# Optimization experiments

Hardware: AMD Instinct MI355X
Metric: run time of the kernel (lower is better)

Reference implementation:

```python
import jax, jax.numpy as jnp
import numpy as np

N_NODES = 100000
N_EDGES = 1600000
IN_CH = 1024
FEAT_CH = 128
OUT_CH = 3


def setup_inputs() -> dict:
    key = jax.random.key(0)
    ks = jax.random.split(key, 9)
    features = jax.random.normal(ks[0], (N_NODES, IN_CH), dtype=jnp.float32)
    edges = jax.random.randint(ks[1], (2, N_EDGES), 0, N_NODES, dtype=jnp.int64)
    edges2 = jax.random.randint(ks[2], (2, N_EDGES), 0, N_NODES, dtype=jnp.int64)
    edge_features = jax.random.normal(ks[3], (N_EDGES, 1), dtype=jnp.float32)
    additional_feature = jax.random.normal(ks[4], (N_NODES, 20), dtype=jnp.float32)
    # GCNConv linear weights (glorot-ish scale) and biases
    W1 = jax.random.normal(ks[5], (IN_CH, FEAT_CH), dtype=jnp.float32) * (1.0 / np.sqrt(IN_CH))
    b1 = jnp.zeros((FEAT_CH,), dtype=jnp.float32)
    W2 = jax.random.normal(ks[6], (FEAT_CH, OUT_CH), dtype=jnp.float32) * (1.0 / np.sqrt(FEAT_CH))
    b2 = jnp.zeros((OUT_CH,), dtype=jnp.float32)
    return {"features": features, "edges": edges, "edges2": edges2,
            "edge_features": edge_features, "additional_feature": additional_feature,
            "W1": W1, "b1": b1, "W2": W2, "b2": b2}


def gcn_conv(x, edge_index, W, b, num_nodes):
    """PyG GCNConv: x' = D^{-1/2}(A+I)D^{-1/2} x W + b (self-loops added)."""
    x = x @ W  # project first (cheaper feature dim for aggregation)
    loop = jnp.arange(num_nodes, dtype=edge_index.dtype)
    src = jnp.concatenate([edge_index[0], loop])
    dst = jnp.concatenate([edge_index[1], loop])
    deg = jax.ops.segment_sum(jnp.ones_like(dst, dtype=x.dtype), dst,
                              num_segments=num_nodes)  # >=1 due to self-loops
    dinv = jax.lax.rsqrt(deg)
    norm = dinv[src] * dinv[dst]  # [E+N]
    out = jax.ops.segment_sum(x[src] * norm[:, None], dst, num_segments=num_nodes)
    return out + b


def reference(features, edges, edges2, edge_features, additional_feature, W1, b1, W2, b2):
    # use_additional_channels=False -> features unchanged; edge_features forced to None
    n = features.shape[0]
    x = gcn_conv(features, edges2, W1, b1, n)
    x = jax.nn.relu(x)
    # dropout inactive in eval mode
    return gcn_conv(x, edges2, W2, b2, n)
```

## Files before the change

### kernel.cpp

```cpp
#include <hip/hip_runtime.h>
#include <hip/hip_bf16.h>

typedef __attribute__((ext_vector_type(8))) _Float16 half8;
typedef __attribute__((ext_vector_type(4))) float f32x4;

#define N_NODES 100000
#define N_EDGES 1600000
#define IN_CH 1024
#define FEAT 128
#define CAP 64
#define NDIG 196
#define CAPC 10240
#define NGB ((N_NODES + 127) / 128)

__device__ __forceinline__ void gload16(const void* g, void* l) {
    __builtin_amdgcn_global_load_lds(
        (const __attribute__((address_space(1))) unsigned int*)g,
        (__attribute__((address_space(3))) unsigned int*)l, 16, 0, 0);
}

#define WAITV(n)                                                               \
    do {                                                                       \
        asm volatile("s_waitcnt vmcnt(" #n ")" ::: "memory");                  \
        __builtin_amdgcn_sched_barrier(0);                                     \
    } while (0)

__global__ void k_prep(const float* __restrict__ W1, _Float16* __restrict__ Bf,
                       int* __restrict__ cursorC, int* __restrict__ done) {
    int idx = blockIdx.x * 256 + threadIdx.x;
    if (idx < IN_CH * FEAT) {
        int col = idx & (FEAT - 1), k = idx >> 7;
        int cf = col >> 4, s = k >> 5;
        int lane = ((k >> 3) & 3) * 16 + (col & 15);
        int e = k & 7;
        Bf[(((cf * 32 + s) * 64 + lane) << 3) + e] = (_Float16)W1[idx];
    }
    if (idx < NDIG) cursorC[idx] = idx * CAPC;
    if (idx == 0) *done = 0;
}

__global__ __launch_bounds__(256, 2) void k_build_gemm(
    const float* __restrict__ A, const _Float16* __restrict__ Bf,
    const int4* __restrict__ src4, const int4* __restrict__ dst4,
    int* __restrict__ cursorC, uint2* __restrict__ recs,
    int* __restrict__ csr, int* __restrict__ cnt, float* __restrict__ dinvarr,
    int* __restrict__ done, _Float16* __restrict__ H, int M, int e4)
{
    __shared__ union {
        float As[16384];
        struct { int hist[NDIG], segoff[NDIG], lcur[NDIG]; } bin;
        int cl[512];
    } sm;
    const int t = threadIdx.x;

    if (blockIdx.x < NDIG) {
        const int b = blockIdx.x;
        if (t < NDIG) sm.bin.hist[t] = 0;
        __syncthreads();
        const int base4 = b * 2048;
        int4 sv[8], dv[8];
#pragma unroll
        for (int j = 0; j < 8; ++j) {
            int idx = base4 + j * 256 + t;
            if (idx < e4) { sv[j] = src4[idx]; dv[j] = dst4[idx]; }
            else { sv[j] = (int4){-1,-1,-1,-1}; dv[j] = (int4){-1,-1,-1,-1}; }
        }
#pragma unroll
        for (int j = 0; j < 8; ++j) {
            int dd[4] = {dv[j].x, dv[j].y, dv[j].z, dv[j].w};
            int ss[4] = {sv[j].x, sv[j].y, sv[j].z, sv[j].w};
#pragma unroll
            for (int c = 0; c < 4; ++c)
                if ((unsigned)dd[c] < N_NODES && (unsigned)ss[c] < N_NODES)
                    atomicAdd(&sm.bin.hist[dd[c] >> 9], 1);
        }
        __syncthreads();
        if (t < NDIG) {
            sm.bin.segoff[t] = atomicAdd(&cursorC[t], sm.bin.hist[t]);
            sm.bin.lcur[t] = 0;
        }
        __syncthreads();
#pragma unroll
        for (int j = 0; j < 8; ++j) {
            int dd[4] = {dv[j].x, dv[j].y, dv[j].z, dv[j].w};
            int ss[4] = {sv[j].x, sv[j].y, sv[j].z, sv[j].w};
#pragma unroll
            for (int c = 0; c < 4; ++c) {
                if ((unsigned)dd[c] < N_NODES && (unsigned)ss[c] < N_NODES) {
                    int dg = dd[c] >> 9;
                    int r = atomicAdd(&sm.bin.lcur[dg], 1);
                    int pos = sm.bin.segoff[dg] + r;
                    if (pos < (dg + 1) * CAPC)
                        recs[pos] = (uint2){(unsigned)ss[c], (unsigned)dd[c]};
                }
            }
        }
        __syncthreads();
        if (t == 0) {
            __threadfence();
            __hip_atomic_fetch_add(done, 1, __ATOMIC_RELEASE, __HIP_MEMORY_SCOPE_AGENT);
            while (__hip_atomic_load(done, __ATOMIC_ACQUIRE, __HIP_MEMORY_SCOPE_AGENT) < NDIG)
                __builtin_amdgcn_s_sleep(8);
        }
        __syncthreads();
        const int d = blockIdx.x;
        for (int j = t; j < 512; j += 256) sm.cl[j] = 0;
        __syncthreads();
        const int base = d * CAPC;
        int n = cursorC[d] - base;
        if (n > CAPC) n = CAPC;
        for (int k = t; k < n; k += 256) {
            uint2 r = recs[base + k];
            int local = (int)r.y & 511;
            int slot = atomicAdd(&sm.cl[local], 1);
            if (slot < CAP) csr[((int)r.y << 6) + slot] = (int)r.x;
        }
        __syncthreads();
        const int node0 = d << 9;
        for (int j = t; j < 512; j += 256) {
            int node = node0 + j;
            if (node < N_NODES) {
                int c = sm.cl[j] < CAP ? sm.cl[j] : CAP;
                cnt[node] = c;
                dinvarr[node] = rsqrtf((float)(c + 1));
            }
        }
        return;
    }

    const int gb = blockIdx.x - NDIG;
    const int brow0 = gb << 7;
    const int wid = t >> 6, lane = t & 63;
    char* ldsw = (char*)sm.As + wid * 16384;

    const char* gsrc[4];
#pragma unroll
    for (int i = 0; i < 4; ++i) {
        int grow = brow0 + wid * 32 + i * 8 + (lane >> 3);
        if (grow >= M) grow = M - 1;
        int gcol = ((lane & 7) * 16) ^ ((lane >> 3) << 4);
        gsrc[i] = (const char*)A + (size_t)grow * 4096 + gcol;
    }
    const _Float16* pbw = Bf + lane * 8;

#define STAGE(bi, ks)                                                           \
    {                                                                           \
        _Pragma("unroll") for (int i = 0; i < 4; ++i)                           \
            gload16(gsrc[i] + (ks) * 128, ldsw + (bi) * 4096 + i * 1024);       \
    }
#define LOADB8(dst, ks)                                                         \
    {                                                                           \
        _Pragma("unroll") for (int cf = 0; cf < 8; ++cf)                        \
            dst[cf] = *(const half8*)(pbw + ((size_t)((cf * 32 + (ks)) << 9))); \
    }
#define MFMA_STEP(bi, bset)                                                     \
    {                                                                           \
        const char* base_ = ldsw + (bi) * 4096;                                 \
        _Pragma("unroll") for (int rf = 0; rf < 2; ++rf) {                      \
            int lr_ = rf * 16 + (lane & 15);                                    \
            int k0_ = (lane >> 4) * 32;                                         \
            int sw_ = (lr_ & 7) << 4;                                           \
            f32x4 lo_ = *(const f32x4*)(base_ + lr_ * 128 + (k0_ ^ sw_));       \
            f32x4 hi_ = *(const f32x4*)(base_ + lr_ * 128 + ((k0_ + 16) ^ sw_));\
            half8 a_;                                                           \
            a_[0] = (_Float16)lo_.x; a_[1] = (_Float16)lo_.y;                   \
            a_[2] = (_Float16)lo_.z; a_[3] = (_Float16)lo_.w;                   \
            a_[4] = (_Float16)hi_.x; a_[5] = (_Float16)hi_.y;                   \
            a_[6] = (_Float16)hi_.z; a_[7] = (_Float16)hi_.w;                   \
            _Pragma("unroll") for (int cf = 0; cf < 8; ++cf)                    \
                acc[rf][cf] = __builtin_amdgcn_mfma_f32_16x16x32_f16(           \
                    a_, bset[cf], acc[rf][cf], 0, 0, 0);                        \
        }                                                                       \
    }

    f32x4 acc[2][8];
#pragma unroll
    for (int rf = 0; rf < 2; ++rf)
#pragma unroll
        for (int cf = 0; cf < 8; ++cf) acc[rf][cf] = (f32x4){0.f, 0.f, 0.f, 0.f};

    half8 bA[8], bB[8];

    STAGE(0, 0); STAGE(1, 1); STAGE(2, 2);
    LOADB8(bA, 0);

#pragma unroll 1
    for (int kt = 0; kt < 32; kt += 2) {
        LOADB8(bB, kt + 1);
        if (kt + 3 < 32) STAGE((kt + 3) & 3, kt + 3);
        if (kt == 0)       WAITV(12);
        else if (kt == 30) WAITV(8);
        else               WAITV(16);
        MFMA_STEP(kt & 3, bA);
        if (kt + 2 < 32) LOADB8(bA, kt + 2);
        if (kt + 4 < 32) STAGE((kt + 4) & 3, kt + 4);
        if (kt == 28)      WAITV(12);
        else if (kt == 30) WAITV(0);
        else               WAITV(16);
        MFMA_STEP((kt + 1) & 3, bB);
    }
#undef STAGE
#undef LOADB8
#undef MFMA_STEP

    {
        int colb = lane & 15, rgrp = (lane >> 4) * 4;
#pragma unroll
        for (int rf = 0; rf < 2; ++rf) {
#pragma unroll
            for (int r = 0; r < 4; ++r) {
                int grow = brow0 + wid * 32 + rf * 16 + rgrp + r;
                if (grow < M) {
                    _Float16* hp = H + (size_t)grow * FEAT + colb;
#pragma unroll
                    for (int cf = 0; cf < 8; ++cf)
                        hp[cf * 16] = (_Float16)acc[rf][cf][r];
                }
            }
        }
    }
}

__global__ __launch_bounds__(256) void k_agg1(const _Float16* __restrict__ H,
                                              const int* __restrict__ csr,
                                              const int* __restrict__ cnt,
                                              const float* __restrict__ dinvarr,
                                              const float* __restrict__ b1,
                                              const float* __restrict__ W2,
                                              float* __restrict__ Y, int n) {
    int wid = threadIdx.x >> 6, lane = threadIdx.x & 63;
    int i = blockIdx.x * 4 + wid;
    if (i >= n) return;
    const int g = lane >> 4, u = lane & 15;
    int m = cnt[i];
    float di = dinvarr[i];

    int sl; float dl;
    if (lane < m) { sl = csr[(i << 6) + lane]; dl = dinvarr[sl]; }
    else          { sl = i;                    dl = (lane == m) ? di : 0.f; }
    int mm = (m < 63 ? m : 63) + 1;

    float ax[8];
#pragma unroll
    for (int j = 0; j < 8; ++j) ax[j] = 0.f;

    for (int e = 0; e < mm; e += 16) {
        int idx0 = e + g, idx1 = e + 4 + g, idx2 = e + 8 + g, idx3 = e + 12 + g;
        bool v0 = idx0 < mm, v1 = idx1 < mm, v2 = idx2 < mm, v3 = idx3 < mm;
        int c0i = v0 ? idx0 : 0, c1i = v1 ? idx1 : 0;
        int c2i = v2 ? idx2 : 0, c3i = v3 ? idx3 : 0;
        int s0 = __shfl(sl, c0i); float w0 = __shfl(dl, c0i);
        int s1 = __shfl(sl, c1i); float w1 = __shfl(dl, c1i);
        int s2 = __shfl(sl, c2i); float w2 = __shfl(dl, c2i);
        int s3 = __shfl(sl, c3i); float w3 = __shfl(dl, c3i);
        if (!v0) { s0 = i; w0 = 0.f; }
        if (!v1) { s1 = i; w1 = 0.f; }
        if (!v2) { s2 = i; w2 = 0.f; }
        if (!v3) { s3 = i; w3 = 0.f; }
        half8 h0 = *(const half8*)(H + ((size_t)s0 << 7) + u * 8);
        half8 h1 = *(const half8*)(H + ((size_t)s1 << 7) + u * 8);
        half8 h2 = *(const half8*)(H + ((size_t)s2 << 7) + u * 8);
        half8 h3 = *(const half8*)(H + ((size_t)s3 << 7) + u * 8);
#pragma unroll
        for (int j = 0; j < 8; ++j)
            ax[j] += w0 * (float)h0[j] + w1 * (float)h1[j]
                   + w2 * (float)h2[j] + w3 * (float)h3[j];
    }

#pragma unroll
    for (int j = 0; j < 8; ++j) {
        ax[j] += __shfl_xor(ax[j], 16);
        ax[j] += __shfl_xor(ax[j], 32);
    }

    int c0 = u * 8;
    float y0 = 0.f, y1 = 0.f, y2 = 0.f;
#pragma unroll
    for (int j = 0; j < 8; ++j) {
        float x = di * ax[j] + b1[c0 + j];
        x = x > 0.f ? x : 0.f;
        y0 += x * W2[(c0 + j) * 3 + 0];
        y1 += x * W2[(c0 + j) * 3 + 1];
        y2 += x * W2[(c0 + j) * 3 + 2];
    }
#pragma unroll
    for (int d = 1; d < 16; d <<= 1) {
        y0 += __shfl_xor(y0, d);
        y1 += __shfl_xor(y1, d);
        y2 += __shfl_xor(y2, d);
    }
    if (lane == 0) {
        float* yp = Y + (size_t)i * 4;
        yp[0] = di * y0; yp[1] = di * y1; yp[2] = di * y2;
    }
}

__global__ void k_agg2(const float* __restrict__ Y, const int* __restrict__ csr,
                       const int* __restrict__ cnt, const float* __restrict__ dinvarr,
                       const float* __restrict__ b2, float* __restrict__ out, int n) {
    int i = blockIdx.x * 256 + threadIdx.x;
    if (i >= n) return;
    int m = cnt[i];
    float di = dinvarr[i];
    int base = i << 6;
    const float4* Y4 = (const float4*)Y;
    float4 self = Y4[i];
    float a0 = self.x, a1 = self.y, a2 = self.z;
    int e = 0;
    for (; e + 3 < m; e += 4) {
        int s0 = csr[base + e],     s1 = csr[base + e + 1];
        int s2 = csr[base + e + 2], s3 = csr[base + e + 3];
        float4 v0 = Y4[s0], v1 = Y4[s1], v2 = Y4[s2], v3 = Y4[s3];
        a0 += (v0.x + v1.x) + (v2.x + v3.x);
        a1 += (v0.y + v1.y) + (v2.y + v3.y);
        a2 += (v0.z + v1.z) + (v2.z + v3.z);
    }
    for (; e < m; ++e) {
        float4 v0 = Y4[csr[base + e]];
        a0 += v0.x; a1 += v0.y; a2 += v0.z;
    }
    out[(size_t)i * 3 + 0] = di * a0 + b2[0];
    out[(size_t)i * 3 + 1] = di * a1 + b2[1];
    out[(size_t)i * 3 + 2] = di * a2 + b2[2];
}

extern "C" void kernel_launch(void* const* d_in, const int* in_sizes, int n_in,
                              void* d_out, int out_size, void* d_ws, size_t ws_size,
                              hipStream_t stream) {
    const float* features = (const float*)d_in[0];
    const int* edges2 = (const int*)d_in[2];
    const float* W1 = (const float*)d_in[5];
    const float* b1 = (const float*)d_in[6];
    const float* W2 = (const float*)d_in[7];
    const float* b2 = (const float*)d_in[8];
    float* out = (float*)d_out;

    const int N = N_NODES, E = N_EDGES;
    const int4* src4 = (const int4*)edges2;
    const int4* dst4 = (const int4*)(edges2 + E);
    int e4 = E / 4;

    char* p = (char*)d_ws;
    auto carve = [&](size_t bytes) { char* q = p; p += (bytes + 255) & ~(size_t)255; return q; };
    int* cnt       = (int*)carve(4 * (size_t)N);
    float* dinvarr = (float*)carve(4 * (size_t)N);
    int* cursorC   = (int*)carve(4 * NDIG);
    int* done      = (int*)carve(4);
    uint2* recs    = (uint2*)carve(8 * (size_t)NDIG * CAPC);
    int* csr       = (int*)carve(4 * (size_t)N * CAP);
    _Float16* Bf   = (_Float16*)carve(2 * (size_t)IN_CH * FEAT);
    _Float16* H    = (_Float16*)carve(2 * (size_t)N * FEAT);
    float* Y       = (float*)carve(16 * (size_t)N);

    k_prep<<<dim3(512), dim3(256), 0, stream>>>(W1, Bf, cursorC, done);
    k_build_gemm<<<dim3(NDIG + NGB), dim3(256), 0, stream>>>(
        features, Bf, src4, dst4, cursorC, recs, csr, cnt, dinvarr, done, H, N, e4);
    k_agg1<<<dim3((N + 3) / 4), dim3(256), 0, stream>>>(H, csr, cnt, dinvarr, b1, W2, Y, N);
    k_agg2<<<dim3((N + 255) / 256), dim3(256), 0, stream>>>(Y, csr, cnt, dinvarr, b2, out, N);
}
```

Baseline: 266.3 us.

## Shrink GEMM tile to 64 rows with double-buffered LDS and block barriers

Reduces the GEMM block tile from 128 rows to 64 rows (16 per wave), shrinking LDS from 64KB to 16KB and raising the occupancy hint from 2 to 3 blocks per CU. The 4-deep per-wave async pipeline with explicit vmcnt waits becomes a 2-buffer scheme with __syncthreads between stages. The aim is more concurrent blocks and more grid parallelism. In exchange each B fragment is reused over fewer rows, B loads double, and the pipeline is shallower with block-wide barriers.

```diff
diff --git a/kernel.cpp b/kernel.cpp
--- a/kernel.cpp
+++ b/kernel.cpp
@@ -11,19 +11,13 @@
 #define CAP 64
 #define NDIG 196
 #define CAPC 10240
-#define NGB ((N_NODES + 127) / 128)
+#define NGB ((N_NODES + 63) / 64)
 
 __device__ __forceinline__ void gload16(const void* g, void* l) {
     __builtin_amdgcn_global_load_lds(
         (const __attribute__((address_space(1))) unsigned int*)g,
         (__attribute__((address_space(3))) unsigned int*)l, 16, 0, 0);
 }
-
-#define WAITV(n)                                                               \
-    do {                                                                       \
-        asm volatile("s_waitcnt vmcnt(" #n ")" ::: "memory");                  \
-        __builtin_amdgcn_sched_barrier(0);                                     \
-    } while (0)
 
 __global__ void k_prep(const float* __restrict__ W1, _Float16* __restrict__ Bf,
                        int* __restrict__ cursorC, int* __restrict__ done) {
@@ -39,7 +33,7 @@
     if (idx == 0) *done = 0;
 }
 
-__global__ __launch_bounds__(256, 2) void k_build_gemm(
+__global__ __launch_bounds__(256, 3) void k_build_gemm(
     const float* __restrict__ A, const _Float16* __restrict__ Bf,
     const int4* __restrict__ src4, const int4* __restrict__ dst4,
     int* __restrict__ cursorC, uint2* __restrict__ recs,
@@ -47,7 +41,7 @@
     int* __restrict__ done, _Float16* __restrict__ H, int M, int e4)
 {
     __shared__ union {
-        float As[16384];
+        float As[4096];
         struct { int hist[NDIG], segoff[NDIG], lcur[NDIG]; } bin;
         int cl[512];
     } sm;
@@ -129,14 +123,13 @@
     }
 
     const int gb = blockIdx.x - NDIG;
-    const int brow0 = gb << 7;
+    const int brow0 = gb << 6;
     const int wid = t >> 6, lane = t & 63;
-    char* ldsw = (char*)sm.As + wid * 16384;
-
-    const char* gsrc[4];
-#pragma unroll
-    for (int i = 0; i < 4; ++i) {
-        int grow = brow0 + wid * 32 + i * 8 + (lane >> 3);
+
+    const char* gsrc[2];
+#pragma unroll
+    for (int i = 0; i < 2; ++i) {
+        int grow = brow0 + wid * 16 + i * 8 + (lane >> 3);
         if (grow >= M) grow = M - 1;
         int gcol = ((lane & 7) * 16) ^ ((lane >> 3) << 4);
         gsrc[i] = (const char*)A + (size_t)grow * 4096 + gcol;
@@ -145,8 +138,9 @@
 
 #define STAGE(bi, ks)                                                           \
     {                                                                           \
-        _Pragma("unroll") for (int i = 0; i < 4; ++i)                           \
-            gload16(gsrc[i] + (ks) * 128, ldsw + (bi) * 4096 + i * 1024);       \
+        _Pragma("unroll") for (int i = 0; i < 2; ++i)                           \
+            gload16(gsrc[i] + (ks) * 128,                                       \
+                    (char*)sm.As + (bi) * 8192 + wid * 2048 + i * 1024);        \
     }
 #define LOADB8(dst, ks)                                                         \
     {                                                                           \
@@ -155,49 +149,48 @@
     }
 #define MFMA_STEP(bi, bset)                                                     \
     {                                                                           \
-        const char* base_ = ldsw + (bi) * 4096;                                 \
-        _Pragma("unroll") for (int rf = 0; rf < 2; ++rf) {                      \
-            int lr_ = rf * 16 + (lane & 15);                                    \
-            int k0_ = (lane >> 4) * 32;                                         \
-            int sw_ = (lr_ & 7) << 4;                                           \
-            f32x4 lo_ = *(const f32x4*)(base_ + lr_ * 128 + (k0_ ^ sw_));       \
-            f32x4 hi_ = *(const f32x4*)(base_ + lr_ * 128 + ((k0_ + 16) ^ sw_));\
-            half8 a_;                                                           \
-            a_[0] = (_Float16)lo_.x; a_[1] = (_Float16)lo_.y;                   \
-            a_[2] = (_Float16)lo_.z; a_[3] = (_Float16)lo_.w;                   \
-            a_[4] = (_Float16)hi_.x; a_[5] = (_Float16)hi_.y;                   \
-            a_[6] = (_Float16)hi_.z; a_[7] = (_Float16)hi_.w;                   \
-            _Pragma("unroll") for (int cf = 0; cf < 8; ++cf)                    \
-                acc[rf][cf] = __builtin_amdgcn_mfma_f32_16x16x32_f16(           \
-                    a_, bset[cf], acc[rf][cf], 0, 0, 0);                        \
-        }                                                                       \
-    }
-
-    f32x4 acc[2][8];
-#pragma unroll
-    for (int rf = 0; rf < 2; ++rf)
-#pragma unroll
-        for (int cf = 0; cf < 8; ++cf) acc[rf][cf] = (f32x4){0.f, 0.f, 0.f, 0.f};
+        const char* base_ = (char*)sm.As + (bi) * 8192;                         \
+        int lr_ = wid * 16 + (lane & 15);                                       \
+        int k0_ = (lane >> 4) * 32;                                             \
+        int sw_ = (lr_ & 7) << 4;                                               \
+        f32x4 lo_ = *(const f32x4*)(base_ + lr_ * 128 + (k0_ ^ sw_));           \
+        f32x4 hi_ = *(const f32x4*)(base_ + lr_ * 128 + ((k0_ + 16) ^ sw_));    \
+        half8 a_;                                                               \
+        a_[0] = (_Float16)lo_.x; a_[1] = (_Float16)lo_.y;                       \
+        a_[2] = (_Float16)lo_.z; a_[3] = (_Float16)lo_.w;                       \
+        a_[4] = (_Float16)hi_.x; a_[5] = (_Float16)hi_.y;                       \
+        a_[6] = (_Float16)hi_.z; a_[7] = (_Float16)hi_.w;                       \
+        _Pragma("unroll") for (int cf = 0; cf < 8; ++cf)                        \
+            acc[cf] = __builtin_amdgcn_mfma_f32_16x16x32_f16(                   \
+                a_, bset[cf], acc[cf], 0, 0, 0);                                \
+    }
+
+    f32x4 acc[8];
+#pragma unroll
+    for (int cf = 0; cf < 8; ++cf) acc[cf] = (f32x4){0.f, 0.f, 0.f, 0.f};
 
     half8 bA[8], bB[8];
 
-    STAGE(0, 0); STAGE(1, 1); STAGE(2, 2);
     LOADB8(bA, 0);
+    STAGE(0, 0);
+    __syncthreads();
 
 #pragma unroll 1
     for (int kt = 0; kt < 32; kt += 2) {
-        LOADB8(bB, kt + 1);
-        if (kt + 3 < 32) STAGE((kt + 3) & 3, kt + 3);
-        if (kt == 0)       WAITV(12);
-        else if (kt == 30) WAITV(8);
-        else               WAITV(16);
-        MFMA_STEP(kt & 3, bA);
-        if (kt + 2 < 32) LOADB8(bA, kt + 2);
-        if (kt + 4 < 32) STAGE((kt + 4) & 3, kt + 4);
-        if (kt == 28)      WAITV(12);
-        else if (kt == 30) WAITV(0);
-        else               WAITV(16);
-        MFMA_STEP((kt + 1) & 3, bB);
+        if (kt + 1 < 32) {
+            LOADB8(bB, kt + 1);
+            STAGE(1, kt + 1);
+        }
+        MFMA_STEP(0, bA);
+        __syncthreads();
+        if (kt + 1 < 32) {
+            if (kt + 2 < 32) {
+                LOADB8(bA, kt + 2);
+                STAGE(0, kt + 2);
+            }
+            MFMA_STEP(1, bB);
+            if (kt + 2 < 32) __syncthreads();
+        }
     }
 #undef STAGE
 #undef LOADB8
@@ -206,16 +199,13 @@
     {
         int colb = lane & 15, rgrp = (lane >> 4) * 4;
 #pragma unroll
-        for (int rf = 0; rf < 2; ++rf) {
-#pragma unroll
-            for (int r = 0; r < 4; ++r) {
-                int grow = brow0 + wid * 32 + rf * 16 + rgrp + r;
-                if (grow < M) {
-                    _Float16* hp = H + (size_t)grow * FEAT + colb;
-#pragma unroll
-                    for (int cf = 0; cf < 8; ++cf)
-                        hp[cf * 16] = (_Float16)acc[rf][cf][r];
-                }
+        for (int r = 0; r < 4; ++r) {
+            int grow = brow0 + wid * 16 + rgrp + r;
+            if (grow < M) {
+                _Float16* hp = H + (size_t)grow * FEAT + colb;
+#pragma unroll
+                for (int cf = 0; cf < 8; ++cf)
+                    hp[cf * 16] = (_Float16)acc[cf][r];
             }
         }
     }
```

Result: slower. 274.0 us (+2.9%).
